# Kernel tuning notes

Measured on AMD Instinct MI355X. Metric: run time of the kernel, lower is better.

Reference implementation:

```python
import jax, jax.numpy as jnp
import numpy as np

POOLED = 7          # square pooled grid (grid_width == grid_height required by torch_combined_meshgrid)
NUM_LEVELS = 6      # len_feature_maps; level = clamp(floor(5 + log2(sqrt(w*h))), 0, 5)


def _bilinear_sample(fm, gx, gy):
    """fm: [C, D, D]; gx, gy: [N, G, G] normalized coords in [0,1].
    Faithful to getWeightedSum_ofFourFmapPoints: floor/ceil corner points with
    proportion weights; coord dim 0 (x) indexes fmap rows, dim 1 (y) indexes cols.
    Returns [N, C, G, G]."""
    D = fm.shape[-1]
    ux = gx * (D - 1)
    uy = gy * (D - 1)
    x0 = jnp.floor(ux); x1 = jnp.ceil(ux)
    y0 = jnp.floor(uy); y1 = jnp.ceil(uy)
    ddx = jnp.where(x1 - x0 == 0, 1.0, x1 - x0)
    ddy = jnp.where(y1 - y0 == 0, 1.0, y1 - y0)
    px0 = 1.0 - (ux - x0) / ddx   # proportion_to_take_from_start_x
    px1 = 1.0 - px0
    py0 = 1.0 - (uy - y0) / ddy
    py1 = 1.0 - py0
    ix0 = x0.astype(jnp.int32); ix1 = x1.astype(jnp.int32)
    iy0 = y0.astype(jnp.int32); iy1 = y1.astype(jnp.int32)
    # advanced indexing: fm[:, idx, idx] -> [C, N, G, G]
    tl = fm[:, ix0, iy0]
    tr = fm[:, ix1, iy0]
    bl = fm[:, ix0, iy1]
    br = fm[:, ix1, iy1]
    w_tl = (px0 * py0)[None]
    w_tr = (px1 * py0)[None]
    w_bl = (px0 * py1)[None]
    w_br = (px1 * py1)[None]
    pooled = w_tl * tl + w_tr * tr + w_bl * bl + w_br * br  # [C, N, G, G]
    return jnp.moveaxis(pooled, 0, 1)                        # [N, C, G, G]


def setup_inputs() -> dict:
    key = jax.random.key(0)
    N, C = 2000, 256
    dims = [38, 19, 10, 5, 3, 1]
    kw, kh, kx, ky, *kf = jax.random.split(key, 4 + len(dims))
    w = jax.random.uniform(kw, (N, 1), minval=0.02, maxval=0.98)
    h = jax.random.uniform(kh, (N, 1), minval=0.02, maxval=0.98)
    x1 = jax.random.uniform(kx, (N, 1)) * (1.0 - w)
    y1 = jax.random.uniform(ky, (N, 1)) * (1.0 - h)
    boxes = jnp.concatenate([x1, y1, x1 + w, y1 + h], axis=1)  # x1 y1 x2 y2 in [0,1]
    out = {"boxes": boxes}
    for i, (d, k) in enumerate(zip(dims, kf)):
        out[f"fmap{i}"] = jax.random.normal(k, (1, C, d, d), dtype=jnp.float32)
    return out


def reference(boxes, fmap0, fmap1, fmap2, fmap3, fmap4, fmap5):
    fmaps = [fmap0, fmap1, fmap2, fmap3, fmap4, fmap5]
    N = boxes.shape[0]
    C = fmap0.shape[1]
    G = POOLED
    x1, y1, x2, y2 = boxes[:, 0:1], boxes[:, 1:2], boxes[:, 2:3], boxes[:, 3:4]
    # FPN-style level index: floor(5 + log2(sqrt(w*h))), clamped (constant w.r.t. grad)
    avg = jnp.sqrt((x2 - x1) * (y2 - y1))
    lvl = jnp.clip(jnp.floor((NUM_LEVELS - 1.0) + jnp.log2(avg)), 0, NUM_LEVELS - 1)
    lvl = jax.lax.stop_gradient(lvl.astype(jnp.int32).reshape(-1))  # [N]
    # bilinear interpolation grid: grid[n,i,j] = (x1 + i*dx/(G-1), y1 + j*dy/(G-1)), clamped
    t = jnp.arange(G, dtype=boxes.dtype)
    denom = max(1.0, G - 1.0)
    xr = jnp.clip(x1 + t[None, :] * (x2 - x1) / denom, 0.0, 1.0)  # [N, G]
    yr = jnp.clip(y1 + t[None, :] * (y2 - y1) / denom, 0.0, 1.0)  # [N, G]
    gx = jnp.broadcast_to(xr[:, :, None], (N, G, G))
    gy = jnp.broadcast_to(yr[:, None, :], (N, G, G))
    out = jnp.zeros((N, C, G, G), dtype=fmap0.dtype)
    for l, f in enumerate(fmaps):
        fm = f[0]  # [C, D, D] (single image; one fmap selected per box)
        if fm.shape[-1] == 1:
            # original returns fmap[:, :, 0:1, 0:1]; broadcast the constant to the grid
            pooled = jnp.broadcast_to(fm[None, :, :1, :1], (N, C, G, G))
        else:
            pooled = _bilinear_sample(fm, gx, gy)
        mask = (lvl == l).astype(fmap0.dtype)[:, None, None, None]
        out = out + mask * pooled
    return out
```

## Files before the change

### kernel.cpp

```cpp
#include <hip/hip_runtime.h>

#define G 7
#define CCH 256
#define NLVL 6

__device__ __constant__ int kD[NLVL]     = {38, 19, 10, 5, 3, 1};
__device__ __constant__ int kD2[NLVL]    = {1444, 361, 100, 25, 9, 1};
__device__ __constant__ int kBaseT[NLVL + 1] = {0, 369664, 462080, 487680, 494080, 496384, 496640};

#define FMT_TOTAL 496640

__global__ __launch_bounds__(256) void transpose_fmaps(
    const float* __restrict__ f0, const float* __restrict__ f1,
    const float* __restrict__ f2, const float* __restrict__ f3,
    const float* __restrict__ f4, const float* __restrict__ f5,
    float* __restrict__ fmT)
{
    int o = blockIdx.x * blockDim.x + threadIdx.x;
    if (o >= FMT_TOTAL) return;
    int l = 0;
#pragma unroll
    for (int k = 1; k < NLVL; ++k) l += (o >= kBaseT[k]);
    int rel = o - kBaseT[l];
    int p = rel >> 8;
    int c = rel & 255;
    const float* f;
    switch (l) {
        case 0: f = f0; break;
        case 1: f = f1; break;
        case 2: f = f2; break;
        case 3: f = f3; break;
        case 4: f = f4; break;
        default: f = f5; break;
    }
    fmT[o] = f[c * kD2[l] + p];
}

__global__ __launch_bounds__(256) void roialign_main(
    const float* __restrict__ boxes, const float* __restrict__ fmT,
    float* __restrict__ out)
{
    __shared__ float4 sOutV[3136];
    __shared__ float4 sW[49];
    __shared__ int4 sOff[49];
    float* sOut = (float*)sOutV;

    int n = blockIdx.x;
    int tid = threadIdx.x;

    if (tid < 49) {
        float bx1 = boxes[n * 4 + 0];
        float by1 = boxes[n * 4 + 1];
        float bx2 = boxes[n * 4 + 2];
        float by2 = boxes[n * 4 + 3];
        float w = bx2 - bx1;
        float h = by2 - by1;
        float avg = sqrtf(w * h);
        float lf = floorf((float)(NLVL - 1) + log2f(avg));
        lf = fminf(fmaxf(lf, 0.0f), (float)(NLVL - 1));
        int lvl = (int)lf;
        int D = kD[lvl];
        float Dm1 = (float)(D - 1);
        int base = kBaseT[lvl];

        int i = tid / 7;
        int j = tid - i * 7;
        float xr = fminf(fmaxf(bx1 + ((float)i * w) / 6.0f, 0.0f), 1.0f);
        float yr = fminf(fmaxf(by1 + ((float)j * h) / 6.0f, 0.0f), 1.0f);
        float ux = xr * Dm1;
        float uy = yr * Dm1;
        float x0 = floorf(ux);
        float y0 = floorf(uy);
        int ix0 = (int)x0;
        int iy0 = (int)y0;
        float fx = ux - x0;
        float fy = uy - y0;
        int ix1 = min(ix0 + 1, D - 1);
        int iy1 = min(iy0 + 1, D - 1);

        sOff[tid] = make_int4(base + (ix0 * D + iy0) * CCH,
                              base + (ix1 * D + iy0) * CCH,
                              base + (ix0 * D + iy1) * CCH,
                              base + (ix1 * D + iy1) * CCH);
        float px0 = 1.0f - fx, py0 = 1.0f - fy;
        sW[tid] = make_float4(px0 * py0, fx * py0, px0 * fy, fx * fy);
    }
    __syncthreads();

#pragma unroll 7
    for (int g = 0; g < 49; ++g) {
        int4 o = sOff[g];
        float4 wv = sW[g];
        float v = wv.x * fmT[o.x + tid] + wv.y * fmT[o.y + tid]
                + wv.z * fmT[o.z + tid] + wv.w * fmT[o.w + tid];
        sOut[tid * 49 + g] = v;
    }
    __syncthreads();

    float4* out4 = (float4*)(out + (size_t)n * (CCH * G * G));
    for (int q = tid; q < 3136; q += 256) out4[q] = sOutV[q];
}

__global__ __launch_bounds__(256) void roialign_fallback(
    const float* __restrict__ boxes,
    const float* __restrict__ f0, const float* __restrict__ f1,
    const float* __restrict__ f2, const float* __restrict__ f3,
    const float* __restrict__ f4, const float* __restrict__ f5,
    float* __restrict__ out, int total4)
{
    int t = blockIdx.x * blockDim.x + threadIdx.x;
    if (t >= total4) return;
    const int perN = CCH * G * G;
    int idx = t * 4;
    int n = idx / perN;
    int rem = idx - n * perN;
    float bx1 = boxes[n * 4 + 0], by1 = boxes[n * 4 + 1];
    float bx2 = boxes[n * 4 + 2], by2 = boxes[n * 4 + 3];
    float w = bx2 - bx1, h = by2 - by1;
    float avg = sqrtf(w * h);
    float lf = floorf((float)(NLVL - 1) + log2f(avg));
    lf = fminf(fmaxf(lf, 0.0f), (float)(NLVL - 1));
    int lvl = (int)lf;
    const float* fm;
    switch (lvl) {
        case 0: fm = f0; break;
        case 1: fm = f1; break;
        case 2: fm = f2; break;
        case 3: fm = f3; break;
        case 4: fm = f4; break;
        default: fm = f5; break;
    }
    int D = kD[lvl];
    float Dm1 = (float)(D - 1);
    float4 res;
    float* rp = &res.x;
#pragma unroll
    for (int k = 0; k < 4; ++k) {
        int e = rem + k;
        int j = e % G;
        int iq = e / G;
        int i = iq % G;
        int c = iq / G;
        float xr = fminf(fmaxf(bx1 + ((float)i * w) / 6.0f, 0.0f), 1.0f);
        float yr = fminf(fmaxf(by1 + ((float)j * h) / 6.0f, 0.0f), 1.0f);
        float ux = xr * Dm1, uy = yr * Dm1;
        float x0 = floorf(ux), y0 = floorf(uy);
        int ix0 = (int)x0, iy0 = (int)y0;
        float fx = ux - x0, fy = uy - y0;
        int ix1 = min(ix0 + 1, D - 1), iy1 = min(iy0 + 1, D - 1);
        const float* p = fm + c * D * D;
        float v00 = p[ix0 * D + iy0], v10 = p[ix1 * D + iy0];
        float v01 = p[ix0 * D + iy1], v11 = p[ix1 * D + iy1];
        float px0 = 1.0f - fx, py0 = 1.0f - fy;
        rp[k] = px0 * py0 * v00 + fx * py0 * v10 + px0 * fy * v01 + fx * fy * v11;
    }
    reinterpret_cast<float4*>(out)[t] = res;
}

extern "C" void kernel_launch(void* const* d_in, const int* in_sizes, int n_in,
                              void* d_out, int out_size, void* d_ws, size_t ws_size,
                              hipStream_t stream) {
    const float* boxes = (const float*)d_in[0];
    const float* f0 = (const float*)d_in[1];
    const float* f1 = (const float*)d_in[2];
    const float* f2 = (const float*)d_in[3];
    const float* f3 = (const float*)d_in[4];
    const float* f4 = (const float*)d_in[5];
    const float* f5 = (const float*)d_in[6];
    float* out = (float*)d_out;
    int N = in_sizes[0] / 4;

    if (ws_size >= (size_t)FMT_TOTAL * sizeof(float)) {
        float* fmT = (float*)d_ws;
        transpose_fmaps<<<(FMT_TOTAL + 255) / 256, 256, 0, stream>>>(
            f0, f1, f2, f3, f4, f5, fmT);
        roialign_main<<<N, 256, 0, stream>>>(boxes, fmT, out);
    } else {
        int total4 = out_size / 4;
        roialign_fallback<<<(total4 + 255) / 256, 256, 0, stream>>>(
            boxes, f0, f1, f2, f3, f4, f5, out, total4);
    }
}
```

Measured before the change: 34.97 us.

## Split each ROI across two blocks by channel half with float2 gathers

```diff
diff --git a/kernel.cpp b/kernel.cpp
--- a/kernel.cpp
+++ b/kernel.cpp
@@ -4,8 +4,8 @@
 #define CCH 256
 #define NLVL 6
 
-__device__ __constant__ int kD[NLVL]     = {38, 19, 10, 5, 3, 1};
-__device__ __constant__ int kD2[NLVL]    = {1444, 361, 100, 25, 9, 1};
+__device__ __constant__ int kD[NLVL]  = {38, 19, 10, 5, 3, 1};
+__device__ __constant__ int kD2[NLVL] = {1444, 361, 100, 25, 9, 1};
 __device__ __constant__ int kBaseT[NLVL + 1] = {0, 369664, 462080, 487680, 494080, 496384, 496640};
 
 #define FMT_TOTAL 496640
@@ -40,12 +40,13 @@
     const float* __restrict__ boxes, const float* __restrict__ fmT,
     float* __restrict__ out)
 {
-    __shared__ float4 sOutV[3136];
+    __shared__ float sOut[128 * 49];
     __shared__ float4 sW[49];
     __shared__ int4 sOff[49];
-    float* sOut = (float*)sOutV;
-
-    int n = blockIdx.x;
+
+    int b = blockIdx.x;
+    int n = b >> 1;
+    int chalf = b & 1;
     int tid = threadIdx.x;
 
     if (tid < 49) {
@@ -87,18 +88,36 @@
     }
     __syncthreads();
 
-#pragma unroll 7
-    for (int g = 0; g < 49; ++g) {
-        int4 o = sOff[g];
-        float4 wv = sW[g];
-        float v = wv.x * fmT[o.x + tid] + wv.y * fmT[o.y + tid]
-                + wv.z * fmT[o.z + tid] + wv.w * fmT[o.w + tid];
-        sOut[tid * 49 + g] = v;
-    }
+    int cpair = tid & 63;
+    int gq = tid >> 6;
+    int cloc = cpair * 2;
+    int cglob = chalf * 128 + cloc;
+    int gBase = gq * 12;
+
+#define BODY(gg)                                                            \
+    {                                                                       \
+        int g = (gg);                                                       \
+        int4 o = sOff[g];                                                   \
+        float4 wv = sW[g];                                                  \
+        float2 a = *(const float2*)(fmT + o.x + cglob);                     \
+        float2 bb = *(const float2*)(fmT + o.y + cglob);                    \
+        float2 cc = *(const float2*)(fmT + o.z + cglob);                    \
+        float2 dd = *(const float2*)(fmT + o.w + cglob);                    \
+        sOut[cloc * 49 + g]       = wv.x * a.x + wv.y * bb.x                \
+                                  + wv.z * cc.x + wv.w * dd.x;              \
+        sOut[(cloc + 1) * 49 + g] = wv.x * a.y + wv.y * bb.y                \
+                                  + wv.z * cc.y + wv.w * dd.y;              \
+    }
+
+#pragma unroll
+    for (int it = 0; it < 12; ++it) BODY(gBase + it);
+    if (gq == 0) BODY(48);
+#undef BODY
     __syncthreads();
 
-    float4* out4 = (float4*)(out + (size_t)n * (CCH * G * G));
-    for (int q = tid; q < 3136; q += 256) out4[q] = sOutV[q];
+    const float4* s4 = (const float4*)sOut;
+    float4* out4 = (float4*)(out + (size_t)n * (CCH * G * G) + chalf * (128 * 49));
+    for (int q = tid; q < 1568; q += 256) out4[q] = s4[q];
 }
 
 __global__ __launch_bounds__(256) void roialign_fallback(
@@ -174,7 +193,7 @@
         float* fmT = (float*)d_ws;
         transpose_fmaps<<<(FMT_TOTAL + 255) / 256, 256, 0, stream>>>(
             f0, f1, f2, f3, f4, f5, fmT);
-        roialign_main<<<N, 256, 0, stream>>>(boxes, fmT, out);
+        roialign_main<<<2 * N, 256, 0, stream>>>(boxes, fmT, out);
     } else {
         int total4 = out_size / 4;
         roialign_fallback<<<(total4 + 255) / 256, 256, 0, stream>>>(
```

Result: slower. 40.25 us (+15.1%).
